# Optimization experiments

Measured on AMD Instinct MI355X. Metric: run time of the kernel, lower is better.

## Reference

```python
import jax, jax.numpy as jnp
import numpy as np
from jax import lax


def setup_inputs() -> dict:
    key = jax.random.key(0)
    kx, kk = jax.random.split(key)
    B, H, W, Cin, Cout, K = 32, 128, 128, 128, 128, 3
    X = jax.random.normal(kx, (B, H, W, Cin), dtype=jnp.float32)
    kernel = jax.random.normal(kk, (B, K, K, Cin, Cout), dtype=jnp.float32)
    return {"X": X, "kernel": kernel}


def reference(X, kernel):
    """Per-sample dynamic conv2d: each batch element gets its own HWIO kernel.

    Equivalent math to the TF depthwise-trick + reduce_sum, but expressed as a
    vmapped standard convolution (fuses the input-channel reduction, avoiding
    the huge [H',W',B*Cin,Cout] intermediate). Padding = 'VALID'.
    """
    dn = ('NHWC', 'HWIO', 'NHWC')

    def conv_one(x, k):
        # x: [H, W, Cin], k: [kh, kw, Cin, Cout] -> [H', W', Cout]
        return lax.conv_general_dilated(
            x[None], k, window_strides=(1, 1), padding='VALID',
            dimension_numbers=dn)[0]

    return jax.vmap(conv_one)(X, kernel)  # [B, H', W', Cout]
```

## Files before the change

### kernel.cpp

```cpp
#include <hip/hip_runtime.h>
#include <stdint.h>

typedef __attribute__((ext_vector_type(8))) short bf16x8;
typedef __attribute__((ext_vector_type(4))) float f32x4;
typedef __attribute__((ext_vector_type(4))) unsigned short u16x4;

#define NB 32
#define HH 128
#define WW 128
#define CI 128
#define CO 128
#define HO 126
#define WO 126
#define TH 16
#define TW 16
#define PHh 18
#define PWw 18
#define NROW (PHh * PWw)
#define RSTR 72
#define RSTRB 144

__device__ __forceinline__ unsigned short f2bf(float f) {
  union { float f; unsigned u; } x; x.f = f;
  unsigned u = x.u;
  u += 0x7FFFu + ((u >> 16) & 1u);
  return (unsigned short)(u >> 16);
}

__device__ __forceinline__ unsigned cvtpk_bf16(float a, float b) {
  unsigned r;
  asm("v_cvt_pk_bf16_f32 %0, %1, %2" : "=v"(r) : "v"(a), "v"(b));
  return r;
}

__global__ void prep_kt(const float* __restrict__ kin, unsigned short* __restrict__ ktr) {
  __shared__ unsigned short t[CI * CO];
  int bp = blockIdx.x;
  int b = bp / 9, p = bp % 9;
  const float* src = kin + (size_t)bp * (CI * CO);
  unsigned short* dstb = ktr + (size_t)b * (9 * CI * CO);
  for (int i = threadIdx.x; i < CI * CO / 4; i += blockDim.x) {
    f32x4 v = *(const f32x4*)(src + i * 4);
    u16x4 o;
    o.x = f2bf(v.x); o.y = f2bf(v.y); o.z = f2bf(v.z); o.w = f2bf(v.w);
    *(u16x4*)&t[i * 4] = o;
  }
  __syncthreads();
  for (int j = threadIdx.x; j < 2048; j += blockDim.x) {
    int lane = j & 63, f = (j >> 6) & 7, sl = j >> 9;
    int ch = sl >> 1, kc = sl & 1;
    int co = (f >> 2) * 64 + (f & 3) * 16 + (lane & 15);
    int ci0 = ch * 64 + kc * 32 + (lane >> 4) * 8;
    bf16x8 v;
#pragma unroll
    for (int e = 0; e < 8; ++e) v[e] = t[(ci0 + e) * CO + co];
    int slice = (ch * 9 + p) * 2 + kc;
    *(bf16x8*)&dstb[(size_t)slice * 4096 + f * 512 + lane * 8] = v;
  }
}

__global__ void conv_naive(const float* __restrict__ X, const float* __restrict__ Kf,
                           float* __restrict__ out) {
  int idx = blockIdx.x * blockDim.x + threadIdx.x;
  if (idx >= NB * HO * WO * CO) return;
  int co = idx & 127, t = idx >> 7;
  int wp = t % WO; t /= WO;
  int hp = t % HO; int b = t / HO;
  const float* xb = X + (size_t)b * HH * WW * CI;
  const float* kb = Kf + (size_t)b * 9 * CI * CO;
  float s = 0.f;
  for (int p = 0; p < 9; ++p) {
    int kh = p / 3, kw = p % 3;
    const float* xr = xb + ((size_t)(hp + kh) * WW + (wp + kw)) * CI;
    const float* kr = kb + (size_t)p * CI * CO + co;
    for (int ci = 0; ci < CI; ++ci) s += xr[ci] * kr[(size_t)ci * CO];
  }
  out[idx] = s;
}

__global__ __launch_bounds__(512, 4) void conv_main(
    const float* __restrict__ X, const unsigned short* __restrict__ Kt,
    float* __restrict__ out) {
  __shared__ unsigned short lds_a[NROW * RSTR];

  const int tid = threadIdx.x;
  const int lane = tid & 63;
  const int wid = tid >> 6;
  const int wr = wid >> 1, wc = wid & 1;

  const int l = blockIdx.x;
  const int xcd = l & 7, j = l >> 3;
  const int b = xcd * 4 + (j >> 6);
  const int t = j & 63;
  const int ht = t >> 3, wt = t & 7;
  const int h0 = ht * TH, w0 = wt * TW;
  const int ks = lane >> 4, lr = lane & 15;

  const float* xb = X + (size_t)b * HH * WW * CI;

  const int ci4 = tid & 15;
  const int row0 = tid >> 4;
  const int hi0 = (row0 >= PWw) ? 1 : 0;
  const int wi0 = row0 - hi0 * PWw;
  char* const dst0 = (char*)lds_a + row0 * RSTRB + ci4 * 8;

  auto stageA = [&](int ch) {
    int h = hi0, w = wi0;
    const float* srcb = xb + ch * 64 + ci4 * 4;
#pragma unroll
    for (int k = 0; k < 11; ++k) {
      if (k < 10 || tid < 64) {
        int gh = h0 + h, gw = w0 + w;
        bool ok = (gh | gw) < HH;
        const float* src = srcb + ((size_t)(((gh & 127) << 7) + (gw & 127)) << 7);
        f32x4 v = *(const f32x4*)src;
        uint2 o;
        o.x = ok ? cvtpk_bf16(v.x, v.y) : 0u;
        o.y = ok ? cvtpk_bf16(v.z, v.w) : 0u;
        *(uint2*)(dst0 + k * (32 * RSTRB)) = o;
      }
      w += 14;
      int wrap = (w >= PWw) ? 1 : 0;
      h += 1 + wrap;
      w -= wrap ? PWw : 0;
    }
  };

  const int aoff = ((wr * 4) * PWw + lr) * RSTRB + ks * 16;
  const char* ldsb = (const char*)lds_a;

  f32x4 zero = {0.f, 0.f, 0.f, 0.f};
  f32x4 acc[4][4];
#pragma unroll
  for (int m = 0; m < 4; ++m)
#pragma unroll
    for (int n = 0; n < 4; ++n) acc[m][n] = zero;

  const unsigned short* ktw = Kt + (size_t)b * 9 * CI * CO + (wc * 4) * 512 + lane * 8;

  bf16x8 Hf[4];
  auto loadBh = [&](int slice) {
#pragma unroll
    for (int n = 0; n < 4; ++n)
      Hf[n] = *(const bf16x8*)&ktw[(size_t)slice * 4096 + n * 512];
  };

#pragma unroll 1
  for (int ch = 0; ch < 2; ++ch) {
    if (ch) __syncthreads();
    loadBh(ch * 18);
    stageA(ch);
    __syncthreads();

#pragma unroll
    for (int kh = 0; kh < 3; ++kh) {
#pragma unroll
      for (int jj = 0; jj < 6; ++jj) {
        const int kw = jj >> 1, kc = jj & 1;
        const int s = kh * 6 + jj;
        bf16x8 af[4];
#pragma unroll
        for (int m = 0; m < 4; ++m)
          af[m] = *(const bf16x8*)(ldsb + aoff +
                                   ((m + kh) * PWw * RSTRB + kw * RSTRB + kc * 64));
        __builtin_amdgcn_s_setprio(1);
#pragma unroll
        for (int m = 0; m < 4; ++m)
#pragma unroll
          for (int n = 0; n < 4; ++n)
            acc[m][n] = __builtin_amdgcn_mfma_f32_16x16x32_bf16(af[m], Hf[n], acc[m][n], 0, 0, 0);
        __builtin_amdgcn_s_setprio(0);
        if (s < 17) loadBh(ch * 18 + s + 1);
      }
    }
  }

  float* ob = out + (size_t)b * HO * WO * CO;
#pragma unroll
  for (int m = 0; m < 4; ++m) {
    int hp = h0 + wr * 4 + m;
    if (hp >= HO) continue;
#pragma unroll
    for (int r = 0; r < 4; ++r) {
      int wp = w0 + ks * 4 + r;
      if (wp >= WO) continue;
#pragma unroll
      for (int n = 0; n < 4; ++n) {
        int co = wc * 64 + n * 16 + lr;
        ob[((size_t)hp * WO + wp) * CO + co] = acc[m][n][r];
      }
    }
  }
}

extern "C" void kernel_launch(void* const* d_in, const int* in_sizes, int n_in,
                              void* d_out, int out_size, void* d_ws, size_t ws_size,
                              hipStream_t stream) {
  const float* X = (const float*)d_in[0];
  const float* Kf = (const float*)d_in[1];
  float* out = (float*)d_out;
  size_t need = (size_t)NB * 9 * CI * CO * sizeof(unsigned short);
  if (d_ws != nullptr && ws_size >= need) {
    unsigned short* ktr = (unsigned short*)d_ws;
    prep_kt<<<dim3(NB * 9), 256, 0, stream>>>(Kf, ktr);
    conv_main<<<dim3(2048), 512, 0, stream>>>(X, ktr, out);
  } else {
    int total = NB * HO * WO * CO;
    conv_naive<<<(total + 255) / 256, 256, 0, stream>>>(X, Kf, out);
  }
}
```

Before: 204.3 us.

## Double-buffer input channel quarters with async global-to-LDS loads overlapping MFMA

Result: slower. 360.7 us (+76.6%).

```diff
diff --git a/kernel.cpp b/kernel.cpp
--- a/kernel.cpp
+++ b/kernel.cpp
@@ -17,8 +17,8 @@
 #define PHh 18
 #define PWw 18
 #define NROW (PHh * PWw)
-#define RSTR 72
-#define RSTRB 144
+#define QSTR 72
+#define QSHORTS (NROW * 36)
 
 __device__ __forceinline__ unsigned short f2bf(float f) {
   union { float f; unsigned u; } x; x.f = f;
@@ -81,7 +81,8 @@
 __global__ __launch_bounds__(512, 4) void conv_main(
     const float* __restrict__ X, const unsigned short* __restrict__ Kt,
     float* __restrict__ out) {
-  __shared__ unsigned short lds_a[NROW * RSTR];
+  __shared__ unsigned short lds_q[2][QSHORTS];
+  __shared__ float ring[1536 * 4];
 
   const int tid = threadIdx.x;
   const int lane = tid & 63;
@@ -96,83 +97,114 @@
   const int h0 = ht * TH, w0 = wt * TW;
   const int ks = lane >> 4, lr = lane & 15;
 
-  const float* xb = X + (size_t)b * HH * WW * CI;
-
-  const int ci4 = tid & 15;
-  const int row0 = tid >> 4;
-  const int hi0 = (row0 >= PWw) ? 1 : 0;
-  const int wi0 = row0 - hi0 * PWw;
-  char* const dst0 = (char*)lds_a + row0 * RSTRB + ci4 * 8;
-
-  auto stageA = [&](int ch) {
-    int h = hi0, w = wi0;
-    const float* srcb = xb + ch * 64 + ci4 * 4;
-#pragma unroll
-    for (int k = 0; k < 11; ++k) {
-      if (k < 10 || tid < 64) {
-        int gh = h0 + h, gw = w0 + w;
-        bool ok = (gh | gw) < HH;
-        const float* src = srcb + ((size_t)(((gh & 127) << 7) + (gw & 127)) << 7);
-        f32x4 v = *(const f32x4*)src;
-        uint2 o;
-        o.x = ok ? cvtpk_bf16(v.x, v.y) : 0u;
-        o.y = ok ? cvtpk_bf16(v.z, v.w) : 0u;
-        *(uint2*)(dst0 + k * (32 * RSTRB)) = o;
-      }
-      w += 14;
-      int wrap = (w >= PWw) ? 1 : 0;
-      h += 1 + wrap;
-      w -= wrap ? PWw : 0;
-    }
+  const char* xb = (const char*)X + ((size_t)b << 23);
+
+  unsigned pofs[6]; unsigned okbits = 0;
+  {
+    int row = tid >> 3;
+    const unsigned g16 = (tid & 7) << 4;
+#pragma unroll
+    for (int k = 0; k < 6; ++k) {
+      int h = row / PWw, w = row - h * PWw;
+      int gh = h0 + h, gw = w0 + w;
+      if ((unsigned)(gh | gw) < 128u) okbits |= (1u << k);
+      pofs[k] = ((unsigned)(((gh & 127) << 7) + (gw & 127)) << 9) + g16;
+      row += 64;
+    }
+  }
+  const int woff = (tid >> 3) * QSTR + ((tid & 7) << 3);
+  const int aoff = ((wr * 4) * PWw + lr) * QSTR + ks * 16;
+
+  char* const q0b = (char*)&lds_q[0][0];
+  char* const q1b = (char*)&lds_q[1][0];
+  char* const ringc = (char*)&ring[0];
+
+  auto fill = [&](int k, int qq) {
+    unsigned roff = (unsigned)(((k % 3) * 512 + wid * 64) * 16);
+    roff = __builtin_amdgcn_readfirstlane(roff);
+    const char* ga = xb + (qq << 7) + pofs[k];
+    __builtin_amdgcn_global_load_lds(
+        (const __attribute__((address_space(1))) void*)ga,
+        (__attribute__((address_space(3))) void*)(ringc + roff), 16, 0, 0);
   };
-
-  const int aoff = ((wr * 4) * PWw + lr) * RSTRB + ks * 16;
-  const char* ldsb = (const char*)lds_a;
-
+  auto cnv = [&](int k, char* wd) {
+    f32x4 v = *(const f32x4*)(ringc + ((k % 3) * 512 + tid) * 16);
+    bool ok = (okbits >> k) & 1;
+    uint2 o;
+    o.x = ok ? cvtpk_bf16(v.x, v.y) : 0u;
+    o.y = ok ? cvtpk_bf16(v.z, v.w) : 0u;
+    *(uint2*)(wd + woff + k * (64 * QSTR)) = o;
+  };
+
+  const unsigned short* ktw = Kt + (size_t)b * 9 * CI * CO + (wc * 4) * 512 + lane * 8;
+  bf16x8 Hf[4];
+  auto loadB = [&](const unsigned short* p) {
+#pragma unroll
+    for (int n = 0; n < 4; ++n)
+      Hf[n] = *(const bf16x8*)(p + n * 512);
+  };
+
+  loadB(ktw);
+#pragma unroll
+  for (int k = 0; k < 6; ++k) {
+    if (k < 5 || tid < 32) {
+      f32x4 v = *(const f32x4*)(xb + pofs[k]);
+      bool ok = (okbits >> k) & 1;
+      uint2 o;
+      o.x = ok ? cvtpk_bf16(v.x, v.y) : 0u;
+      o.y = ok ? cvtpk_bf16(v.z, v.w) : 0u;
+      *(uint2*)(q0b + woff + k * (64 * QSTR)) = o;
+    }
+  }
   f32x4 zero = {0.f, 0.f, 0.f, 0.f};
   f32x4 acc[4][4];
 #pragma unroll
   for (int m = 0; m < 4; ++m)
 #pragma unroll
     for (int n = 0; n < 4; ++n) acc[m][n] = zero;
-
-  const unsigned short* ktw = Kt + (size_t)b * 9 * CI * CO + (wc * 4) * 512 + lane * 8;
-
-  bf16x8 Hf[4];
-  auto loadBh = [&](int slice) {
-#pragma unroll
-    for (int n = 0; n < 4; ++n)
-      Hf[n] = *(const bf16x8*)&ktw[(size_t)slice * 4096 + n * 512];
-  };
+  __syncthreads();
 
 #pragma unroll 1
-  for (int ch = 0; ch < 2; ++ch) {
-    if (ch) __syncthreads();
-    loadBh(ch * 18);
-    stageA(ch);
-    __syncthreads();
-
-#pragma unroll
-    for (int kh = 0; kh < 3; ++kh) {
-#pragma unroll
-      for (int jj = 0; jj < 6; ++jj) {
-        const int kw = jj >> 1, kc = jj & 1;
-        const int s = kh * 6 + jj;
-        bf16x8 af[4];
-#pragma unroll
-        for (int m = 0; m < 4; ++m)
-          af[m] = *(const bf16x8*)(ldsb + aoff +
-                                   ((m + kh) * PWw * RSTRB + kw * RSTRB + kc * 64));
-        __builtin_amdgcn_s_setprio(1);
-#pragma unroll
-        for (int m = 0; m < 4; ++m)
-#pragma unroll
-          for (int n = 0; n < 4; ++n)
-            acc[m][n] = __builtin_amdgcn_mfma_f32_16x16x32_bf16(af[m], Hf[n], acc[m][n], 0, 0, 0);
-        __builtin_amdgcn_s_setprio(0);
-        if (s < 17) loadBh(ch * 18 + s + 1);
-      }
-    }
+  for (int q = 0; q < 4; ++q) {
+    const char* rb = (q & 1) ? q1b : q0b;
+    char* wd = (q & 1) ? q0b : q1b;
+    const unsigned short* bq = ktw + (size_t)((q >> 1) * 18 + (q & 1)) * 4096;
+    const unsigned short* bnext =
+        ktw + (size_t)(((q + 1) >> 1) * 18 + ((q + 1) & 1)) * 4096;
+    const bool stg = (q < 3);
+#pragma unroll
+    for (int p = 0; p < 9; ++p) {
+      if (stg) {
+        if (p < 3) fill(p, q + 1);
+        else if (p >= 5 && p < 8) {
+          if (p < 7 || tid < 32) fill(p - 2, q + 1);
+        }
+      }
+      const int kh = p / 3, kw = p % 3;
+      bf16x8 af[4];
+#pragma unroll
+      for (int m = 0; m < 4; ++m)
+        af[m] = *(const bf16x8*)(rb + aoff + (((m + kh) * PWw + kw) * QSTR));
+      __builtin_amdgcn_s_setprio(1);
+#pragma unroll
+      for (int m = 0; m < 4; ++m)
+#pragma unroll
+        for (int n = 0; n < 4; ++n)
+          acc[m][n] = __builtin_amdgcn_mfma_f32_16x16x32_bf16(af[m], Hf[n], acc[m][n], 0, 0, 0);
+      __builtin_amdgcn_s_setprio(0);
+      if (p < 8) loadB(bq + (size_t)(p + 1) * 8192);
+      else if (stg) loadB(bnext);
+      if (stg && p == 4) {
+        asm volatile("s_waitcnt vmcnt(2)" ::: "memory");
+        cnv(0, wd); cnv(1, wd); cnv(2, wd);
+      }
+      if (stg && p == 8) {
+        asm volatile("s_waitcnt vmcnt(2)" ::: "memory");
+        cnv(3, wd); cnv(4, wd);
+        if (tid < 32) cnv(5, wd);
+      }
+    }
+    if (q < 3) __syncthreads();
   }
 
   float* ob = out + (size_t)b * HO * WO * CO;
```

## Pre-convert input to bf16 and double-buffer LDS staging via direct global-to-LDS loads

Applied to the files above, without the earlier changes.

Result: slower. 276.5 us (+35.3%).

```diff
diff --git a/kernel.cpp b/kernel.cpp
--- a/kernel.cpp
+++ b/kernel.cpp
@@ -4,6 +4,7 @@
 typedef __attribute__((ext_vector_type(8))) short bf16x8;
 typedef __attribute__((ext_vector_type(4))) float f32x4;
 typedef __attribute__((ext_vector_type(4))) unsigned short u16x4;
+typedef __attribute__((ext_vector_type(4))) unsigned int u32x4;
 
 #define NB 32
 #define HH 128
@@ -19,6 +20,10 @@
 #define NROW (PHh * PWw)
 #define RSTR 72
 #define RSTRB 144
+#define ZOFF 9437184u
+#define XOFF 9438208u
+#define QROWS 336
+#define QBYTES (QROWS * 64)
 
 __device__ __forceinline__ unsigned short f2bf(float f) {
   union { float f; unsigned u; } x; x.f = f;
@@ -56,6 +61,24 @@
     for (int e = 0; e < 8; ++e) v[e] = t[(ci0 + e) * CO + co];
     int slice = (ch * 9 + p) * 2 + kc;
     *(bf16x8*)&dstb[(size_t)slice * 4096 + f * 512 + lane * 8] = v;
+  }
+}
+
+__global__ void prep_x(const float* __restrict__ X, char* __restrict__ ws) {
+  if (blockIdx.x == 0 && threadIdx.x < 256)
+    ((unsigned*)(ws + ZOFF))[threadIdx.x] = 0u;
+  unsigned short* xb = (unsigned short*)(ws + XOFF);
+  const int total = NB * HH * WW * CI / 8;
+  int stride = gridDim.x * blockDim.x;
+  for (int i = blockIdx.x * blockDim.x + threadIdx.x; i < total; i += stride) {
+    f32x4 a = *(const f32x4*)(X + (size_t)i * 8);
+    f32x4 c = *(const f32x4*)(X + (size_t)i * 8 + 4);
+    u32x4 o;
+    o.x = cvtpk_bf16(a.x, a.y);
+    o.y = cvtpk_bf16(a.z, a.w);
+    o.z = cvtpk_bf16(c.x, c.y);
+    o.w = cvtpk_bf16(c.z, c.w);
+    *(u32x4*)(xb + (size_t)i * 8) = o;
   }
 }
 
@@ -78,10 +101,9 @@
   out[idx] = s;
 }
 
-__global__ __launch_bounds__(512, 4) void conv_main(
-    const float* __restrict__ X, const unsigned short* __restrict__ Kt,
-    float* __restrict__ out) {
-  __shared__ unsigned short lds_a[NROW * RSTR];
+__global__ __launch_bounds__(512, 4) void conv_main_bf(
+    const char* __restrict__ ws, float* __restrict__ out) {
+  __shared__ char lds_q[2][QBYTES];
 
   const int tid = threadIdx.x;
   const int lane = tid & 63;
@@ -96,8 +118,121 @@
   const int h0 = ht * TH, w0 = wt * TW;
   const int ks = lane >> 4, lr = lane & 15;
 
+  unsigned pofs[3];
+  {
+    const unsigned xbo = XOFF + ((unsigned)b << 22);
+#pragma unroll
+    for (int k = 0; k < 3; ++k) {
+      int jj = wid + k * 8;
+      int row = jj * 16 + (lane >> 2);
+      int c = lane & 3;
+      int h = row / PWw, w = row - h * PWw;
+      int gh = h0 + h, gw = w0 + w;
+      bool ok = (row < NROW) && ((unsigned)(gh | gw) < 128u);
+      pofs[k] = ok ? xbo + ((unsigned)(((gh & 127) << 7) + (gw & 127)) << 8) + (c << 4)
+                   : ZOFF + (unsigned)(c << 4);
+    }
+  }
+  auto stageQ = [&](int q, int buf) {
+#pragma unroll
+    for (int k = 0; k < 3; ++k) {
+      int jj = wid + k * 8;
+      if (jj < 21) {
+        unsigned lo = (unsigned)(buf * QBYTES + jj * 1024);
+        lo = __builtin_amdgcn_readfirstlane(lo);
+        const char* ga = ws + pofs[k] + (q << 6);
+        __builtin_amdgcn_global_load_lds(
+            (const __attribute__((address_space(1))) void*)ga,
+            (__attribute__((address_space(3))) void*)(&lds_q[0][0] + lo), 16, 0, 0);
+      }
+    }
+  };
+
+  const int aoff = ((wr * 4) * PWw + lr) * 64 + ks * 16;
+
+  const unsigned short* ktw = (const unsigned short*)ws +
+                              (size_t)b * 9 * CI * CO + (wc * 4) * 512 + lane * 8;
+  bf16x8 Hf[4];
+  auto loadB = [&](const unsigned short* p) {
+#pragma unroll
+    for (int n = 0; n < 4; ++n)
+      Hf[n] = *(const bf16x8*)(p + n * 512);
+  };
+
+  f32x4 zero = {0.f, 0.f, 0.f, 0.f};
+  f32x4 acc[4][4];
+#pragma unroll
+  for (int m = 0; m < 4; ++m)
+#pragma unroll
+    for (int n = 0; n < 4; ++n) acc[m][n] = zero;
+
+  stageQ(0, 0);
+  loadB(ktw);
+  __syncthreads();
+
+#pragma unroll 1
+  for (int q = 0; q < 4; ++q) {
+    const char* rb = &lds_q[q & 1][0];
+    const unsigned short* bq = ktw + (size_t)((q >> 1) * 18 + (q & 1)) * 4096;
+    const unsigned short* bnext =
+        ktw + (size_t)(((q + 1) >> 1) * 18 + ((q + 1) & 1)) * 4096;
+#pragma unroll
+    for (int p = 0; p < 9; ++p) {
+      const int kh = p / 3, kw = p % 3;
+      bf16x8 af[4];
+#pragma unroll
+      for (int m = 0; m < 4; ++m)
+        af[m] = *(const bf16x8*)(rb + aoff + ((m + kh) * PWw + kw) * 64);
+      __builtin_amdgcn_s_setprio(1);
+#pragma unroll
+      for (int m = 0; m < 4; ++m)
+#pragma unroll
+        for (int n = 0; n < 4; ++n)
+          acc[m][n] = __builtin_amdgcn_mfma_f32_16x16x32_bf16(af[m], Hf[n], acc[m][n], 0, 0, 0);
+      __builtin_amdgcn_s_setprio(0);
+      if (p < 8) loadB(bq + (size_t)(p + 1) * 8192);
+      else if (q < 3) loadB(bnext);
+      if (p == 0 && q < 3) stageQ(q + 1, (q & 1) ^ 1);
+    }
+    if (q < 3) __syncthreads();
+  }
+
+  float* ob = out + (size_t)b * HO * WO * CO;
+#pragma unroll
+  for (int m = 0; m < 4; ++m) {
+    int hp = h0 + wr * 4 + m;
+    if (hp >= HO) continue;
+#pragma unroll
+    for (int r = 0; r < 4; ++r) {
+      int wp = w0 + ks * 4 + r;
+      if (wp >= WO) continue;
+#pragma unroll
+      for (int n = 0; n < 4; ++n) {
+        int co = wc * 64 + n * 16 + lr;
+        ob[((size_t)hp * WO + wp) * CO + co] = acc[m][n][r];
+      }
+    }
+  }
+}
+
+__global__ __launch_bounds__(512, 4) void conv_main(
+    const float* __restrict__ X, const unsigned short* __restrict__ Kt,
+    float* __restrict__ out) {
+  __shared__ unsigned short lds_a[NROW * RSTR];
+
+  const int tid = threadIdx.x;
+  const int lane = tid & 63;
+  const int wid = tid >> 6;
+  const int wr = wid >> 1, wc = wid & 1;
+  const int l = blockIdx.x;
+  const int xcd = l & 7, j = l >> 3;
+  const int b = xcd * 4 + (j >> 6);
+  const int t = j & 63;
+  const int ht = t >> 3, wt = t & 7;
+  const int h0 = ht * TH, w0 = wt * TW;
+  const int ks = lane >> 4, lr = lane & 15;
+
   const float* xb = X + (size_t)b * HH * WW * CI;
-
   const int ci4 = tid & 15;
   const int row0 = tid >> 4;
   const int hi0 = (row0 >= PWw) ? 1 : 0;
@@ -137,7 +272,6 @@
     for (int n = 0; n < 4; ++n) acc[m][n] = zero;
 
   const unsigned short* ktw = Kt + (size_t)b * 9 * CI * CO + (wc * 4) * 512 + lane * 8;
-
   bf16x8 Hf[4];
   auto loadBh = [&](int slice) {
 #pragma unroll
@@ -151,7 +285,6 @@
     loadBh(ch * 18);
     stageA(ch);
     __syncthreads();
-
 #pragma unroll
     for (int kh = 0; kh < 3; ++kh) {
 #pragma unroll
@@ -199,8 +332,14 @@
   const float* X = (const float*)d_in[0];
   const float* Kf = (const float*)d_in[1];
   float* out = (float*)d_out;
-  size_t need = (size_t)NB * 9 * CI * CO * sizeof(unsigned short);
-  if (d_ws != nullptr && ws_size >= need) {
+  size_t need_small = (size_t)NB * 9 * CI * CO * sizeof(unsigned short);
+  size_t need_big = (size_t)XOFF + (size_t)NB * HH * WW * CI * 2;
+  if (d_ws != nullptr && ws_size >= need_big) {
+    char* ws = (char*)d_ws;
+    prep_kt<<<dim3(NB * 9), 256, 0, stream>>>(Kf, (unsigned short*)ws);
+    prep_x<<<dim3(4096), 256, 0, stream>>>(X, ws);
+    conv_main_bf<<<dim3(2048), 512, 0, stream>>>(ws, out);
+  } else if (d_ws != nullptr && ws_size >= need_small) {
     unsigned short* ktr = (unsigned short*)d_ws;
     prep_kt<<<dim3(NB * 9), 256, 0, stream>>>(Kf, ktr);
     conv_main<<<dim3(2048), 512, 0, stream>>>(X, ktr, out);
```

## Halve spatial tile to 8x16 with 256 threads and double-buffer LDS A fragments

Applied to the files above, without the earlier changes.

Result: slower. 232.2 us (+13.6%).

```diff
diff --git a/kernel.cpp b/kernel.cpp
--- a/kernel.cpp
+++ b/kernel.cpp
@@ -12,9 +12,9 @@
 #define CO 128
 #define HO 126
 #define WO 126
-#define TH 16
+#define TH 8
 #define TW 16
-#define PHh 18
+#define PHh 10
 #define PWw 18
 #define NROW (PHh * PWw)
 #define RSTR 72
@@ -78,7 +78,7 @@
   out[idx] = s;
 }
 
-__global__ __launch_bounds__(512, 4) void conv_main(
+__global__ __launch_bounds__(256, 3) void conv_main(
     const float* __restrict__ X, const unsigned short* __restrict__ Kt,
     float* __restrict__ out) {
   __shared__ unsigned short lds_a[NROW * RSTR];
@@ -90,8 +90,8 @@
 
   const int l = blockIdx.x;
   const int xcd = l & 7, j = l >> 3;
-  const int b = xcd * 4 + (j >> 6);
-  const int t = j & 63;
+  const int b = xcd * 4 + (j >> 7);
+  const int t = j & 127;
   const int ht = t >> 3, wt = t & 7;
   const int h0 = ht * TH, w0 = wt * TW;
   const int ks = lane >> 4, lr = lane & 15;
@@ -100,16 +100,14 @@
 
   const int ci4 = tid & 15;
   const int row0 = tid >> 4;
-  const int hi0 = (row0 >= PWw) ? 1 : 0;
-  const int wi0 = row0 - hi0 * PWw;
   char* const dst0 = (char*)lds_a + row0 * RSTRB + ci4 * 8;
 
   auto stageA = [&](int ch) {
-    int h = hi0, w = wi0;
+    int h = 0, w = row0;
     const float* srcb = xb + ch * 64 + ci4 * 4;
 #pragma unroll
-    for (int k = 0; k < 11; ++k) {
-      if (k < 10 || tid < 64) {
+    for (int k = 0; k < 12; ++k) {
+      if (k < 11 || tid < 64) {
         int gh = h0 + h, gw = w0 + w;
         bool ok = (gh | gw) < HH;
         const float* src = srcb + ((size_t)(((gh & 127) << 7) + (gw & 127)) << 7);
@@ -117,12 +115,10 @@
         uint2 o;
         o.x = ok ? cvtpk_bf16(v.x, v.y) : 0u;
         o.y = ok ? cvtpk_bf16(v.z, v.w) : 0u;
-        *(uint2*)(dst0 + k * (32 * RSTRB)) = o;
-      }
-      w += 14;
-      int wrap = (w >= PWw) ? 1 : 0;
-      h += 1 + wrap;
-      w -= wrap ? PWw : 0;
+        *(uint2*)(dst0 + k * (16 * RSTRB)) = o;
+      }
+      w += 16;
+      if (w >= PWw) { w -= PWw; h += 1; }
     }
   };
 
@@ -137,12 +133,30 @@
     for (int n = 0; n < 4; ++n) acc[m][n] = zero;
 
   const unsigned short* ktw = Kt + (size_t)b * 9 * CI * CO + (wc * 4) * 512 + lane * 8;
-
   bf16x8 Hf[4];
   auto loadBh = [&](int slice) {
 #pragma unroll
     for (int n = 0; n < 4; ++n)
       Hf[n] = *(const bf16x8*)&ktw[(size_t)slice * 4096 + n * 512];
+  };
+
+  bf16x8 afA[4], afB[4];
+  auto issueAf = [&](bf16x8 (&dst)[4], int s) {
+    const int kh = s / 6, jj = s % 6;
+    const int kw = jj >> 1, kc = jj & 1;
+#pragma unroll
+    for (int m = 0; m < 4; ++m)
+      dst[m] = *(const bf16x8*)(ldsb + aoff +
+                                ((m + kh) * PWw * RSTRB + kw * RSTRB + kc * 64));
+  };
+  auto mma = [&](bf16x8 (&use)[4]) {
+    __builtin_amdgcn_s_setprio(1);
+#pragma unroll
+    for (int m = 0; m < 4; ++m)
+#pragma unroll
+      for (int n = 0; n < 4; ++n)
+        acc[m][n] = __builtin_amdgcn_mfma_f32_16x16x32_bf16(use[m], Hf[n], acc[m][n], 0, 0, 0);
+    __builtin_amdgcn_s_setprio(0);
   };
 
 #pragma unroll 1
@@ -151,25 +165,19 @@
     loadBh(ch * 18);
     stageA(ch);
     __syncthreads();
-
-#pragma unroll
-    for (int kh = 0; kh < 3; ++kh) {
-#pragma unroll
-      for (int jj = 0; jj < 6; ++jj) {
-        const int kw = jj >> 1, kc = jj & 1;
-        const int s = kh * 6 + jj;
-        bf16x8 af[4];
-#pragma unroll
-        for (int m = 0; m < 4; ++m)
-          af[m] = *(const bf16x8*)(ldsb + aoff +
-                                   ((m + kh) * PWw * RSTRB + kw * RSTRB + kc * 64));
-        __builtin_amdgcn_s_setprio(1);
-#pragma unroll
-        for (int m = 0; m < 4; ++m)
-#pragma unroll
-          for (int n = 0; n < 4; ++n)
-            acc[m][n] = __builtin_amdgcn_mfma_f32_16x16x32_bf16(af[m], Hf[n], acc[m][n], 0, 0, 0);
-        __builtin_amdgcn_s_setprio(0);
+    issueAf(afA, 0);
+#pragma unroll
+    for (int u = 0; u < 9; ++u) {
+      {
+        const int s = 2 * u;
+        issueAf(afB, s + 1);
+        mma(afA);
+        loadBh(ch * 18 + s + 1);
+      }
+      {
+        const int s = 2 * u + 1;
+        if (s < 17) issueAf(afA, s + 1);
+        mma(afB);
         if (s < 17) loadBh(ch * 18 + s + 1);
       }
     }
@@ -203,7 +211,7 @@
   if (d_ws != nullptr && ws_size >= need) {
     unsigned short* ktr = (unsigned short*)d_ws;
     prep_kt<<<dim3(NB * 9), 256, 0, stream>>>(Kf, ktr);
-    conv_main<<<dim3(2048), 512, 0, stream>>>(X, ktr, out);
+    conv_main<<<dim3(4096), 256, 0, stream>>>(X, ktr, out);
   } else {
     int total = NB * HO * WO * CO;
     conv_naive<<<(total + 255) / 256, 256, 0, stream>>>(X, Kf, out);
```
